# Kernel tuning notes

Measured on AMD Instinct MI355X. Metric: run time of the kernel, lower is better.

Reference implementation:

```python
import jax, jax.numpy as jnp
import numpy as np

T, B, S = 50, 64, 100
H, C = 512, 512
V_TGT, V_EXT = 32000, 5000
UNK = 0  # ext_dict.stoi[UNK_WORD]


def setup_inputs() -> dict:
    key = jax.random.key(0)
    ks = jax.random.split(key, 8)
    return {
        "hidden": jax.random.normal(ks[0], (T, B, H), jnp.float32),
        "dec_rnn_output": jax.random.normal(ks[1], (T, B, H), jnp.float32),
        "concat_c": jax.random.normal(ks[2], (T, B, H + C), jnp.float32),
        "attn": jax.random.uniform(ks[3], (T, B, S), jnp.float32),
        "copy_to_ext": jax.random.randint(ks[4], (S, B), 0, V_EXT, jnp.int64),
        "W": jax.random.normal(ks[5], (V_TGT, H), jnp.float32) * 0.02,
        "b": jnp.zeros((V_TGT,), jnp.float32),
        "Wc": jax.random.normal(ks[6], (1, H), jnp.float32) * 0.02,
        "bc": jnp.zeros((1,), jnp.float32),
    }


def _safe_log(v):
    return jnp.log(jnp.clip(v, 0.001, 1.0 - 0.001))


def reference(hidden, dec_rnn_output, concat_c, attn, copy_to_ext, W, b, Wc, bc):
    # standard softmax over tgt vocab
    logits = jnp.einsum("tbh,vh->tbv", hidden, W) + b          # [T,B,V_TGT]
    prob_log = jax.nn.log_softmax(logits, axis=-1)
    # copy gate p(z) from decoder hidden (copy_prb == 'hidden')
    copy = jax.nn.sigmoid(jnp.einsum("tbh,oh->tbo", dec_rnn_output, Wc) + bc)  # [T,B,1]
    mul_attn = attn * (1.0 - copy)                              # [T,B,S]
    # onehot+bmm == masked scatter-add of attn mass into ext-vocab bins
    mask = (copy_to_ext != UNK).astype(mul_attn.dtype)          # [S,B]
    aw = mul_attn * mask.T[None]                                # [T,B,S]

    def scatter_one(a_ts, idx_s):  # a_ts [T,S], idx_s [S]
        return jnp.zeros((T, V_EXT), a_ts.dtype).at[:, idx_s].add(a_ts)

    ext_copy_prob = jax.vmap(scatter_one, in_axes=(1, 1), out_axes=1)(aw, copy_to_ext)  # [T,B,V_EXT]
    ext_copy_prob_log = _safe_log(ext_copy_prob)
    return jnp.concatenate([prob_log, ext_copy_prob_log], axis=-1)  # [T,B,V_TGT+V_EXT]
```

## Files before the change

kernel.cpp:

```cpp
#include <hip/hip_runtime.h>
#include <hip/hip_bf16.h>

#define TT 50
#define BB 64
#define SS 100
#define HH 512
#define VT 32000
#define VE 5000
#define LDC 37000
#define MROWS 3200
#define NTILE 250
#define TSTR 136

typedef __bf16 bf16x8 __attribute__((ext_vector_type(8)));
typedef float f32x4 __attribute__((ext_vector_type(4)));

__device__ __forceinline__ ushort f2bf(float f) {
    unsigned u = __float_as_uint(f);
    u += 0x7fffu + ((u >> 16) & 1u);
    return (ushort)(u >> 16);
}
__device__ __forceinline__ float bflo(unsigned u) { return __uint_as_float(u << 16); }
__device__ __forceinline__ float bfhi(unsigned u) { return __uint_as_float(u & 0xffff0000u); }

__global__ void convert_kernel(const float* __restrict__ W, const float* __restrict__ hid,
                               ushort* __restrict__ wsB, ushort* __restrict__ wsA) {
    int g = blockIdx.x * 256 + threadIdx.x;
    const int WG = 4096000;
    float4 v;
    ushort* dst;
    if (g < WG) {
        v = ((const float4*)W)[g];
        dst = wsB + 4 * (size_t)g;
    } else {
        int h = g - WG;
        v = ((const float4*)hid)[h];
        dst = wsA + 4 * (size_t)h;
    }
    ushort4 o;
    o.x = f2bf(v.x); o.y = f2bf(v.y); o.z = f2bf(v.z); o.w = f2bf(v.w);
    *(ushort4*)dst = o;
}

__global__ void gemm_kernel(const ushort* __restrict__ A, const ushort* __restrict__ B,
                            const float* __restrict__ bias, ushort* __restrict__ outu,
                            float* __restrict__ pm, float* __restrict__ ps) {
    __shared__ ushort lds[8192];
    __shared__ ushort tileT[128 * TSTR];
    const int tid  = threadIdx.x;
    const int w    = tid >> 6;
    const int lane = tid & 63;
    const int wr   = w >> 1, wc = w & 1;
    const int brow = blockIdx.y * 128;
    const int bcol = blockIdx.x * 128;
    const int lr   = lane & 15;
    const int kg   = lane >> 4;

    char* ldsAb = (char*)lds;
    char* ldsBb = (char*)lds + 8192;

    f32x4 acc[4][4];
#pragma unroll
    for (int m = 0; m < 4; ++m)
#pragma unroll
        for (int n = 0; n < 4; ++n)
            acc[m][n] = (f32x4){0.f, 0.f, 0.f, 0.f};

    for (int kt = 0; kt < 16; ++kt) {
        __syncthreads();
#pragma unroll
        for (int j = 0; j < 2; ++j) {
            int c = tid + j * 256;
            int row = c >> 2, kc = c & 3;
            const ushort* srcA = A + (size_t)(brow + row) * HH + kt * 32 + kc * 8;
            __builtin_amdgcn_global_load_lds(
                (const __attribute__((address_space(1))) void*)srcA,
                (__attribute__((address_space(3))) void*)(ldsAb + (w * 64 + j * 256) * 16),
                16, 0, 0);
            const ushort* srcB = B + (size_t)(bcol + row) * HH + kt * 32 + kc * 8;
            __builtin_amdgcn_global_load_lds(
                (const __attribute__((address_space(1))) void*)srcB,
                (__attribute__((address_space(3))) void*)(ldsBb + (w * 64 + j * 256) * 16),
                16, 0, 0);
        }
        __syncthreads();

        bf16x8 af[4], bfr[4];
#pragma unroll
        for (int m = 0; m < 4; ++m)
            af[m] = *(const bf16x8*)(ldsAb + ((wr * 64 + m * 16 + lr) * 64 + kg * 16));
#pragma unroll
        for (int n = 0; n < 4; ++n)
            bfr[n] = *(const bf16x8*)(ldsBb + ((wc * 64 + n * 16 + lr) * 64 + kg * 16));
#pragma unroll
        for (int m = 0; m < 4; ++m)
#pragma unroll
            for (int n = 0; n < 4; ++n)
                acc[m][n] = __builtin_amdgcn_mfma_f32_16x16x32_bf16(af[m], bfr[n], acc[m][n], 0, 0, 0);
    }

#pragma unroll
    for (int n = 0; n < 4; ++n) {
        int col = wc * 64 + n * 16 + lr;
        float bv = bias[bcol + col];
#pragma unroll
        for (int m = 0; m < 4; ++m) {
            int row0 = wr * 64 + m * 16 + kg * 4;
#pragma unroll
            for (int r = 0; r < 4; ++r)
                tileT[(row0 + r) * TSTR + col] = f2bf(acc[m][n][r] + bv);
        }
    }
    __syncthreads();

#pragma unroll
    for (int it = 0; it < 8; ++it) {
        int idx = it * 256 + tid;
        int row = idx >> 4, ch = idx & 15;
        uint4 v = *(const uint4*)(&tileT[row * TSTR + ch * 8]);
        *(uint4*)(outu + (size_t)(brow + row) * 74000 + 42000 + bcol + ch * 8) = v;
    }

    {
        int prow = tid >> 1, half = tid & 1;
        const ushort* trow = &tileT[prow * TSTR + half * 64];
        uint4 vv[8];
#pragma unroll
        for (int i = 0; i < 8; ++i) vv[i] = *(const uint4*)(trow + i * 8);
        float mx = -1e30f;
#pragma unroll
        for (int i = 0; i < 8; ++i) {
            mx = fmaxf(mx, fmaxf(fmaxf(bflo(vv[i].x), bfhi(vv[i].x)), fmaxf(bflo(vv[i].y), bfhi(vv[i].y))));
            mx = fmaxf(mx, fmaxf(fmaxf(bflo(vv[i].z), bfhi(vv[i].z)), fmaxf(bflo(vv[i].w), bfhi(vv[i].w))));
        }
        float sx = 0.f;
#pragma unroll
        for (int i = 0; i < 8; ++i) {
            sx += __expf(bflo(vv[i].x) - mx) + __expf(bfhi(vv[i].x) - mx)
                + __expf(bflo(vv[i].y) - mx) + __expf(bfhi(vv[i].y) - mx)
                + __expf(bflo(vv[i].z) - mx) + __expf(bfhi(vv[i].z) - mx)
                + __expf(bflo(vv[i].w) - mx) + __expf(bfhi(vv[i].w) - mx);
        }
        float om = __shfl_xor(mx, 1), os = __shfl_xor(sx, 1);
        float M = fmaxf(mx, om);
        float S = sx * __expf(mx - M) + os * __expf(om - M);
        if (half == 0) {
            pm[(size_t)blockIdx.x * MROWS + brow + prow] = M;
            ps[(size_t)blockIdx.x * MROWS + brow + prow] = S;
        }
    }
}

__global__ __launch_bounds__(512) void norm_kernel(float* __restrict__ out,
                                                   const float* __restrict__ pm,
                                                   const float* __restrict__ ps) {
    const int r = blockIdx.x;
    const int t = threadIdx.x;
    __shared__ float sm[8], ssum[8];
    __shared__ float lse_sh;
    __shared__ ushort rowbuf[VT];

    float m = -1e30f, s = 0.f;
    if (t < NTILE) {
        m = pm[(size_t)t * MROWS + r];
        s = ps[(size_t)t * MROWS + r];
    }
    for (int off = 1; off < 64; off <<= 1) {
        float om = __shfl_xor(m, off), os = __shfl_xor(s, off);
        float nm = fmaxf(m, om);
        s = s * __expf(m - nm) + os * __expf(om - nm);
        m = nm;
    }
    int w = t >> 6, lane = t & 63;
    if (lane == 0) { sm[w] = m; ssum[w] = s; }

    const uint4* src = (const uint4*)((const ushort*)out + (size_t)r * 74000 + 42000);
    uint4* dstl = (uint4*)rowbuf;
    for (int i = t; i < VT / 8; i += 512) dstl[i] = src[i];
    __syncthreads();

    if (t == 0) {
        float M = sm[0], S = ssum[0];
        for (int i = 1; i < 8; ++i) {
            float nm = fmaxf(M, sm[i]);
            S = S * __expf(M - nm) + ssum[i] * __expf(sm[i] - nm);
            M = nm;
        }
        lse_sh = M + __logf(S);
    }
    __syncthreads();
    const float l = lse_sh;

    float4* orow = (float4*)(out + (size_t)r * LDC);
    for (int i = t; i < VT / 8; i += 512) {
        uint4 v = dstl[i];
        float4 a, b;
        a.x = bflo(v.x) - l; a.y = bfhi(v.x) - l;
        a.z = bflo(v.y) - l; a.w = bfhi(v.y) - l;
        b.x = bflo(v.z) - l; b.y = bfhi(v.z) - l;
        b.z = bflo(v.w) - l; b.w = bfhi(v.w) - l;
        orow[2 * i]     = a;
        orow[2 * i + 1] = b;
    }
}

__global__ void ext_kernel(float* __restrict__ out, const float* __restrict__ dec,
                           const float* __restrict__ wc, const float* __restrict__ bcp,
                           const float* __restrict__ attn, const int* __restrict__ cte) {
    const int r = blockIdx.x;
    const int t = threadIdx.x;
    __shared__ float red[4];
    __shared__ float cshare;
    __shared__ float bins[VE];

    const float* d = dec + (size_t)r * HH;
    float part = d[t] * wc[t] + d[t + 256] * wc[t + 256];
    for (int off = 1; off < 64; off <<= 1) part += __shfl_xor(part, off);
    int w = t >> 6, lane = t & 63;
    if (lane == 0) red[w] = part;
    for (int v = t; v < VE; v += 256) bins[v] = 0.f;
    __syncthreads();
    if (t == 0) {
        float g = red[0] + red[1] + red[2] + red[3] + bcp[0];
        cshare = 1.f / (1.f + __expf(-g));
    }
    __syncthreads();
    float c = cshare;

    if (t < SS) {
        float aw = attn[(size_t)r * SS + t] * (1.f - c);
        int idx = cte[t * BB + (r & 63)];
        if (idx != 0) atomicAdd(&bins[idx], aw);
    }
    __syncthreads();

    float4* eo = (float4*)(out + (size_t)r * LDC + VT);
    for (int v = t; v < VE / 4; v += 256) {
        float4 x;
        x.x = __logf(fminf(fmaxf(bins[4 * v + 0], 0.001f), 0.999f));
        x.y = __logf(fminf(fmaxf(bins[4 * v + 1], 0.001f), 0.999f));
        x.z = __logf(fminf(fmaxf(bins[4 * v + 2], 0.001f), 0.999f));
        x.w = __logf(fminf(fmaxf(bins[4 * v + 3], 0.001f), 0.999f));
        eo[v] = x;
    }
}

extern "C" void kernel_launch(void* const* d_in, const int* in_sizes, int n_in,
                              void* d_out, int out_size, void* d_ws, size_t ws_size,
                              hipStream_t stream) {
    const float* hidden = (const float*)d_in[0];
    const float* dec    = (const float*)d_in[1];
    const float* attn   = (const float*)d_in[3];
    const int*   cte    = (const int*)d_in[4];
    const float* W      = (const float*)d_in[5];
    const float* bias   = (const float*)d_in[6];
    const float* Wc     = (const float*)d_in[7];
    const float* bc     = (const float*)d_in[8];
    float* out = (float*)d_out;

    ushort* wsB = (ushort*)d_ws;
    ushort* wsA = wsB + (size_t)VT * HH;
    float*  pm  = (float*)(wsA + (size_t)MROWS * HH);
    float*  ps  = pm + (size_t)NTILE * MROWS;

    convert_kernel<<<17600, 256, 0, stream>>>(W, hidden, wsB, wsA);
    gemm_kernel<<<dim3(NTILE, 25), 256, 0, stream>>>(wsA, wsB, bias, (ushort*)out, pm, ps);
    norm_kernel<<<MROWS, 512, 0, stream>>>(out, pm, ps);
    ext_kernel<<<MROWS, 256, 0, stream>>>(out, dec, Wc, bc, attn, cte);
}
```

Measured before the change: 368.8 us.

## Double GEMM K-tile with XOR-swizzled LDS, fuse norm and ext-copy kernels

The GEMM now loads 64-wide K slices per iteration (8 iterations instead of 16), which halves the barrier count. It XOR-swizzles the LDS layout to avoid bank conflicts and reuses the staging buffer for the epilogue tile. The norm and ext-copy kernels are merged into one 512-thread kernel, dropping a launch and rereading of shared state. To fit LDS alongside the 5000 bins, only part of each row is staged, and the remainder of the 32000-column output is read directly from global memory. The fused kernel carries some odd no-op writes, and the staging split adds a read-after-write dependence on the aliased output region.

```diff
diff --git a/kernel.cpp b/kernel.cpp
--- a/kernel.cpp
+++ b/kernel.cpp
@@ -11,6 +11,7 @@
 #define MROWS 3200
 #define NTILE 250
 #define TSTR 136
+#define STG_COLS 22016
 
 typedef __bf16 bf16x8 __attribute__((ext_vector_type(8)));
 typedef float f32x4 __attribute__((ext_vector_type(4)));
@@ -45,8 +46,7 @@
 __global__ void gemm_kernel(const ushort* __restrict__ A, const ushort* __restrict__ B,
                             const float* __restrict__ bias, ushort* __restrict__ outu,
                             float* __restrict__ pm, float* __restrict__ ps) {
-    __shared__ ushort lds[8192];
-    __shared__ ushort tileT[128 * TSTR];
+    __shared__ char smem[34816];
     const int tid  = threadIdx.x;
     const int w    = tid >> 6;
     const int lane = tid & 63;
@@ -56,8 +56,9 @@
     const int lr   = lane & 15;
     const int kg   = lane >> 4;
 
-    char* ldsAb = (char*)lds;
-    char* ldsBb = (char*)lds + 8192;
+    char* ldsAb = smem;
+    char* ldsBb = smem + 16384;
+    ushort* tileT = (ushort*)smem;
 
     f32x4 acc[4][4];
 #pragma unroll
@@ -66,38 +67,44 @@
         for (int n = 0; n < 4; ++n)
             acc[m][n] = (f32x4){0.f, 0.f, 0.f, 0.f};
 
-    for (int kt = 0; kt < 16; ++kt) {
+    for (int kt = 0; kt < 8; ++kt) {
         __syncthreads();
 #pragma unroll
-        for (int j = 0; j < 2; ++j) {
+        for (int j = 0; j < 4; ++j) {
             int c = tid + j * 256;
-            int row = c >> 2, kc = c & 3;
-            const ushort* srcA = A + (size_t)(brow + row) * HH + kt * 32 + kc * 8;
+            int row = c >> 3, kc = c & 7;
+            int kcs = kc ^ (row & 7);
+            const ushort* srcA = A + (size_t)(brow + row) * HH + kt * 64 + kcs * 8;
             __builtin_amdgcn_global_load_lds(
                 (const __attribute__((address_space(1))) void*)srcA,
-                (__attribute__((address_space(3))) void*)(ldsAb + (w * 64 + j * 256) * 16),
+                (__attribute__((address_space(3))) void*)(ldsAb + c * 16),
                 16, 0, 0);
-            const ushort* srcB = B + (size_t)(bcol + row) * HH + kt * 32 + kc * 8;
+            const ushort* srcB = B + (size_t)(bcol + row) * HH + kt * 64 + kcs * 8;
             __builtin_amdgcn_global_load_lds(
                 (const __attribute__((address_space(1))) void*)srcB,
-                (__attribute__((address_space(3))) void*)(ldsBb + (w * 64 + j * 256) * 16),
+                (__attribute__((address_space(3))) void*)(ldsBb + c * 16),
                 16, 0, 0);
         }
         __syncthreads();
 
-        bf16x8 af[4], bfr[4];
-#pragma unroll
-        for (int m = 0; m < 4; ++m)
-            af[m] = *(const bf16x8*)(ldsAb + ((wr * 64 + m * 16 + lr) * 64 + kg * 16));
-#pragma unroll
-        for (int n = 0; n < 4; ++n)
-            bfr[n] = *(const bf16x8*)(ldsBb + ((wc * 64 + n * 16 + lr) * 64 + kg * 16));
-#pragma unroll
-        for (int m = 0; m < 4; ++m)
+#pragma unroll
+        for (int s = 0; s < 2; ++s) {
+            bf16x8 af[4], bfr[4];
+            int xof = ((s * 4 + kg) ^ (lr & 7)) << 4;
+#pragma unroll
+            for (int m = 0; m < 4; ++m)
+                af[m] = *(const bf16x8*)(ldsAb + (wr * 64 + m * 16 + lr) * 128 + xof);
 #pragma unroll
             for (int n = 0; n < 4; ++n)
-                acc[m][n] = __builtin_amdgcn_mfma_f32_16x16x32_bf16(af[m], bfr[n], acc[m][n], 0, 0, 0);
-    }
+                bfr[n] = *(const bf16x8*)(ldsBb + (wc * 64 + n * 16 + lr) * 128 + xof);
+#pragma unroll
+            for (int m = 0; m < 4; ++m)
+#pragma unroll
+                for (int n = 0; n < 4; ++n)
+                    acc[m][n] = __builtin_amdgcn_mfma_f32_16x16x32_bf16(af[m], bfr[n], acc[m][n], 0, 0, 0);
+        }
+    }
+    __syncthreads();
 
 #pragma unroll
     for (int n = 0; n < 4; ++n) {
@@ -151,14 +158,20 @@
     }
 }
 
-__global__ __launch_bounds__(512) void norm_kernel(float* __restrict__ out,
-                                                   const float* __restrict__ pm,
-                                                   const float* __restrict__ ps) {
+__global__ __launch_bounds__(512) void norm_ext_kernel(float* __restrict__ out,
+                                                       const float* __restrict__ pm,
+                                                       const float* __restrict__ ps,
+                                                       const float* __restrict__ dec,
+                                                       const float* __restrict__ wc,
+                                                       const float* __restrict__ bcp,
+                                                       const float* __restrict__ attn,
+                                                       const int* __restrict__ cte) {
     const int r = blockIdx.x;
     const int t = threadIdx.x;
     __shared__ float sm[8], ssum[8];
-    __shared__ float lse_sh;
-    __shared__ ushort rowbuf[VT];
+    __shared__ float lse_sh, csh;
+    __shared__ ushort stg[STG_COLS];
+    __shared__ float bins[VE];
 
     float m = -1e30f, s = 0.f;
     if (t < NTILE) {
@@ -174,26 +187,39 @@
     int w = t >> 6, lane = t & 63;
     if (lane == 0) { sm[w] = m; ssum[w] = s; }
 
-    const uint4* src = (const uint4*)((const ushort*)out + (size_t)r * 74000 + 42000);
-    uint4* dstl = (uint4*)rowbuf;
-    for (int i = t; i < VT / 8; i += 512) dstl[i] = src[i];
-    __syncthreads();
-
-    if (t == 0) {
-        float M = sm[0], S = ssum[0];
-        for (int i = 1; i < 8; ++i) {
-            float nm = fmaxf(M, sm[i]);
-            S = S * __expf(M - nm) + ssum[i] * __expf(sm[i] - nm);
-            M = nm;
-        }
-        lse_sh = M + __logf(S);
+    {
+        float part = dec[(size_t)r * HH + t] * wc[t];
+        for (int off = 1; off < 64; off <<= 1) part += __shfl_xor(part, off);
+        if (lane == 0) ssum[w] += 0.f, sm[w] += 0.f;
+        __shared__ float red[8];
+        if (lane == 0) red[w] = part;
+        if (t == 0) csh = 0.f;
+        const uint4* src = (const uint4*)((const ushort*)out + (size_t)r * 74000 + 42000);
+        uint4* dstl = (uint4*)stg;
+        for (int i = t; i < STG_COLS / 8; i += 512) dstl[i] = src[i];
+        for (int v = t; v < VE; v += 512) bins[v] = 0.f;
+        __syncthreads();
+        if (t == 0) {
+            float M = sm[0], S = ssum[0];
+            for (int i = 1; i < 8; ++i) {
+                float nm = fmaxf(M, sm[i]);
+                S = S * __expf(M - nm) + ssum[i] * __expf(sm[i] - nm);
+                M = nm;
+            }
+            lse_sh = M + __logf(S);
+            float g = red[0] + red[1] + red[2] + red[3]
+                    + red[4] + red[5] + red[6] + red[7] + bcp[0];
+            csh = 1.f / (1.f + __expf(-g));
+        }
     }
     __syncthreads();
     const float l = lse_sh;
 
+    const uint4* gsrc = (const uint4*)((const ushort*)out + (size_t)r * 74000 + 42000);
+    const uint4* lsrc = (const uint4*)stg;
     float4* orow = (float4*)(out + (size_t)r * LDC);
     for (int i = t; i < VT / 8; i += 512) {
-        uint4 v = dstl[i];
+        uint4 v = (i < STG_COLS / 8) ? lsrc[i] : gsrc[i];
         float4 a, b;
         a.x = bflo(v.x) - l; a.y = bfhi(v.x) - l;
         a.z = bflo(v.y) - l; a.w = bfhi(v.y) - l;
@@ -202,40 +228,16 @@
         orow[2 * i]     = a;
         orow[2 * i + 1] = b;
     }
-}
-
-__global__ void ext_kernel(float* __restrict__ out, const float* __restrict__ dec,
-                           const float* __restrict__ wc, const float* __restrict__ bcp,
-                           const float* __restrict__ attn, const int* __restrict__ cte) {
-    const int r = blockIdx.x;
-    const int t = threadIdx.x;
-    __shared__ float red[4];
-    __shared__ float cshare;
-    __shared__ float bins[VE];
-
-    const float* d = dec + (size_t)r * HH;
-    float part = d[t] * wc[t] + d[t + 256] * wc[t + 256];
-    for (int off = 1; off < 64; off <<= 1) part += __shfl_xor(part, off);
-    int w = t >> 6, lane = t & 63;
-    if (lane == 0) red[w] = part;
-    for (int v = t; v < VE; v += 256) bins[v] = 0.f;
-    __syncthreads();
-    if (t == 0) {
-        float g = red[0] + red[1] + red[2] + red[3] + bcp[0];
-        cshare = 1.f / (1.f + __expf(-g));
-    }
-    __syncthreads();
-    float c = cshare;
 
     if (t < SS) {
-        float aw = attn[(size_t)r * SS + t] * (1.f - c);
+        float aw = attn[(size_t)r * SS + t] * (1.f - csh);
         int idx = cte[t * BB + (r & 63)];
         if (idx != 0) atomicAdd(&bins[idx], aw);
     }
     __syncthreads();
 
     float4* eo = (float4*)(out + (size_t)r * LDC + VT);
-    for (int v = t; v < VE / 4; v += 256) {
+    for (int v = t; v < VE / 4; v += 512) {
         float4 x;
         x.x = __logf(fminf(fmaxf(bins[4 * v + 0], 0.001f), 0.999f));
         x.y = __logf(fminf(fmaxf(bins[4 * v + 1], 0.001f), 0.999f));
@@ -265,6 +267,5 @@
 
     convert_kernel<<<17600, 256, 0, stream>>>(W, hidden, wsB, wsA);
     gemm_kernel<<<dim3(NTILE, 25), 256, 0, stream>>>(wsA, wsB, bias, (ushort*)out, pm, ps);
-    norm_kernel<<<MROWS, 512, 0, stream>>>(out, pm, ps);
-    ext_kernel<<<MROWS, 256, 0, stream>>>(out, dec, Wc, bc, attn, cte);
-}
+    norm_ext_kernel<<<MROWS, 512, 0, stream>>>(out, pm, ps, dec, Wc, bc, attn, cte);
+}
```

Result: no change. 372.1 us (+0.9%).
